# Kernel optimization log

Hardware: AMD Instinct MI355X
Metric: run time of the kernel (lower is better)

Reference implementation:

```python
import jax, jax.numpy as jnp
import numpy as np

N_NODES = 50000
N_EDGES = 800000
ENC_DIM = 128


def setup_inputs() -> dict:
    key = jax.random.key(0)
    k_h, k_s, k_d, k_w1, k_w2 = jax.random.split(key, 5)
    h = jax.random.normal(k_h, (N_NODES, ENC_DIM), dtype=jnp.float32)
    edge_src = jax.random.randint(k_s, (N_EDGES,), 0, N_NODES, dtype=jnp.int32)
    edge_dst = jax.random.randint(k_d, (N_EDGES,), 0, N_NODES, dtype=jnp.int32)
    # Linear(enc_dim*2 -> enc_dim) per layer; scaled init for numerical sanity
    scale = 1.0 / np.sqrt(2 * ENC_DIM)
    W1 = jax.random.normal(k_w1, (2 * ENC_DIM, ENC_DIM), dtype=jnp.float32) * scale
    b1 = jnp.zeros((ENC_DIM,), dtype=jnp.float32)
    W2 = jax.random.normal(k_w2, (2 * ENC_DIM, ENC_DIM), dtype=jnp.float32) * scale
    b2 = jnp.zeros((ENC_DIM,), dtype=jnp.float32)
    return {"h": h, "edge_src": edge_src, "edge_dst": edge_dst,
            "W1": W1, "b1": b1, "W2": W2, "b2": b2}


def _sage_layer(h, edge_src, edge_dst, W, b):
    # mean over neighbor features: segment-sum messages h[src] at dst, divide by degree
    n = h.shape[0]
    msg_sum = jax.ops.segment_sum(h[edge_src], edge_dst, num_segments=n)  # [N, D]
    deg = jax.ops.segment_sum(jnp.ones_like(edge_dst, dtype=h.dtype), edge_dst,
                              num_segments=n)  # [N]
    m = msg_sum / jnp.maximum(deg, 1.0)[:, None]  # zero-neighbor nodes -> zeros
    hc = jnp.concatenate([h, m], axis=1)  # [N, 2D]
    return jax.nn.relu(hc @ W + b)


def reference(h, edge_src, edge_dst, W1, b1, W2, b2):
    h = _sage_layer(h, edge_src, edge_dst, W1, b1)
    h = _sage_layer(h, edge_src, edge_dst, W2, b2)
    return h
```

## Files before the change

kernel.cpp:

```cpp
#include <hip/hip_runtime.h>

#define D 128
#define BKT_SHIFT 9
#define BKT_NODES 512
#define NBK 128
#define CHUNK 2048
#define CAP 12288

typedef short short8 __attribute__((ext_vector_type(8)));
typedef float f32x4  __attribute__((ext_vector_type(4)));

__device__ __forceinline__ unsigned short f2bf(float f) {
    unsigned int u = __builtin_bit_cast(unsigned int, f);
    u += 0x7FFFu + ((u >> 16) & 1u);
    return (unsigned short)(u >> 16);
}
__device__ __forceinline__ float bflo(unsigned int u) {
    return __builtin_bit_cast(float, u << 16);
}
__device__ __forceinline__ float bfhi(unsigned int u) {
    return __builtin_bit_cast(float, u & 0xFFFF0000u);
}

__global__ __launch_bounds__(256) void prep_bucket(
    const float* __restrict__ h, unsigned short* __restrict__ hbf, int n8,
    int hblocks,
    const float* __restrict__ W1, const float* __restrict__ W2,
    unsigned short* __restrict__ wf1, unsigned short* __restrict__ wf2,
    const int* __restrict__ esrc, const int* __restrict__ edst,
    int* __restrict__ cursor, int* __restrict__ adj_st, int n_edges)
{
    const int bid = blockIdx.x;
    const int tid = threadIdx.x;
    if (bid < hblocks) {
        const int t = bid * 256 + tid;
        if (t >= n8) return;
        const float4 a = reinterpret_cast<const float4*>(h)[t * 2];
        const float4 b = reinterpret_cast<const float4*>(h)[t * 2 + 1];
        union { short8 s; unsigned short u[8]; } pk;
        pk.u[0]=f2bf(a.x); pk.u[1]=f2bf(a.y); pk.u[2]=f2bf(a.z); pk.u[3]=f2bf(a.w);
        pk.u[4]=f2bf(b.x); pk.u[5]=f2bf(b.y); pk.u[6]=f2bf(b.z); pk.u[7]=f2bf(b.w);
        reinterpret_cast<short8*>(hbf)[t] = pk.s;
    } else if (bid < hblocks + 32) {
        const int t = (bid - hblocks) * 256 + tid;
        const int which = t >> 12;
        const int u = t & 4095;
        const float* W = which ? W2 : W1;
        unsigned short* wf = which ? wf2 : wf1;
        const int lane = u & 63;
        const int frag = u >> 6;
        const int ctb  = frag >> 3;
        const int kc   = frag & 7;
        const int col  = ctb * 16 + (lane & 15);
        const int k0   = kc * 32 + (lane >> 4) * 8;
        unsigned short o[8];
        #pragma unroll
        for (int j = 0; j < 8; ++j) o[j] = f2bf(W[(size_t)(k0 + j) * D + col]);
        #pragma unroll
        for (int j = 0; j < 8; ++j) wf[(size_t)u * 8 + j] = o[j];
    } else {
        __shared__ int lcnt[NBK], lbase[NBK];
        const int base = (bid - hblocks - 32) * CHUNK;
        if (tid < NBK) lcnt[tid] = 0;
        __syncthreads();
        int d[8], s[8], loc[8];
        #pragma unroll
        for (int k = 0; k < 8; ++k) {
            const int i = base + k * 256 + tid;
            if (i < n_edges) {
                d[k] = edst[i]; s[k] = esrc[i];
                loc[k] = atomicAdd(&lcnt[d[k] >> BKT_SHIFT], 1);
            }
        }
        __syncthreads();
        if (tid < NBK)
            lbase[tid] = tid * CAP +
                (lcnt[tid] ? atomicAdd(&cursor[tid], lcnt[tid]) : 0);
        __syncthreads();
        #pragma unroll
        for (int k = 0; k < 8; ++k) {
            const int i = base + k * 256 + tid;
            if (i < n_edges) {
                const int b = d[k] >> BKT_SHIFT;
                adj_st[lbase[b] + loc[k]] = (int)(
                    ((unsigned int)(d[k] & (BKT_NODES - 1)) << 16) |
                    (unsigned int)s[k]);
            }
        }
    }
}

__global__ __launch_bounds__(256) void bucket_fill(
    const int* __restrict__ cursor, int* __restrict__ adj_st,
    int* __restrict__ row_start, int* __restrict__ deg, int n_nodes)
{
    __shared__ unsigned int lbuf[CAP];
    __shared__ int cnt[BKT_NODES], pref[BKT_NODES], cur[BKT_NODES];
    __shared__ int wsum[4];
    const int b   = blockIdx.x;
    const int tid = threadIdx.x;
    const int nb  = min(cursor[b], CAP);
    const int s0  = b * CAP;

    for (int i = tid; i < nb; i += 256) lbuf[i] = (unsigned int)adj_st[s0 + i];
    for (int i = tid; i < BKT_NODES; i += 256) cnt[i] = 0;
    __syncthreads();
    for (int i = tid; i < nb; i += 256)
        atomicAdd(&cnt[lbuf[i] >> 16], 1);
    __syncthreads();

    const int lane = tid & 63, w = tid >> 6;
    const int v0 = cnt[2 * tid], v1 = cnt[2 * tid + 1];
    const int sv = v0 + v1;
    int incl = sv;
    #pragma unroll
    for (int off = 1; off < 64; off <<= 1) {
        int t = __shfl_up(incl, off, 64);
        if (lane >= off) incl += t;
    }
    if (lane == 63) wsum[w] = incl;
    __syncthreads();
    int wp = 0;
    #pragma unroll
    for (int k = 0; k < 4; ++k) if (k < w) wp += wsum[k];
    const int ex = wp + incl - sv;
    pref[2 * tid] = ex;           cur[2 * tid] = 0;
    pref[2 * tid + 1] = ex + v0;  cur[2 * tid + 1] = 0;
    __syncthreads();

    for (int r = tid; r < BKT_NODES; r += 256) {
        const int node = b * BKT_NODES + r;
        if (node < n_nodes) { row_start[node] = s0 + pref[r]; deg[node] = cnt[r]; }
    }

    for (int i = tid; i < nb; i += 256) {
        const unsigned int p = lbuf[i];
        const int r = p >> 16;
        adj_st[s0 + pref[r] + atomicAdd(&cur[r], 1)] = (int)(p & 0xFFFFu);
    }
}

__global__ __launch_bounds__(256) void gather_sort(
    const unsigned short* __restrict__ hbf, int* __restrict__ adj,
    const int* __restrict__ row_start, const int* __restrict__ deg,
    unsigned short* __restrict__ msgbf, int n_nodes)
{
    const int lane = threadIdx.x & 63;
    const int node = (blockIdx.x * 256 + threadIdx.x) >> 6;
    if (node >= n_nodes) return;
    const unsigned int* h2 = reinterpret_cast<const unsigned int*>(hbf);

    const int s0 = row_start[node];
    const int d  = deg[node];
    float ax0=0.f, ay0=0.f, ax1=0.f, ay1=0.f, ax2=0.f, ay2=0.f, ax3=0.f, ay3=0.f;
    float ax4=0.f, ay4=0.f, ax5=0.f, ay5=0.f, ax6=0.f, ay6=0.f, ax7=0.f, ay7=0.f;

    if (d <= 64) {
        int v = (lane < d) ? adj[s0 + lane] : 0x7FFFFFFF;
        if (d > 1) {
            #pragma unroll
            for (int k = 2; k <= 64; k <<= 1) {
                #pragma unroll
                for (int j = k >> 1; j >= 1; j >>= 1) {
                    const int p = __shfl_xor(v, j, 64);
                    const bool keepMin = (((lane & k) == 0) == ((lane & j) == 0));
                    v = keepMin ? (v < p ? v : p) : (v > p ? v : p);
                }
            }
            if (lane < d) adj[s0 + lane] = v;
        }
        int p = 0;
        for (; p + 7 < d; p += 8) {
            const int i0 = __shfl(v, p),     i1 = __shfl(v, p + 1);
            const int i2 = __shfl(v, p + 2), i3 = __shfl(v, p + 3);
            const int i4 = __shfl(v, p + 4), i5 = __shfl(v, p + 5);
            const int i6 = __shfl(v, p + 6), i7 = __shfl(v, p + 7);
            const unsigned int w0 = h2[(size_t)i0 * 64 + lane];
            const unsigned int w1 = h2[(size_t)i1 * 64 + lane];
            const unsigned int w2 = h2[(size_t)i2 * 64 + lane];
            const unsigned int w3 = h2[(size_t)i3 * 64 + lane];
            const unsigned int w4 = h2[(size_t)i4 * 64 + lane];
            const unsigned int w5 = h2[(size_t)i5 * 64 + lane];
            const unsigned int w6 = h2[(size_t)i6 * 64 + lane];
            const unsigned int w7 = h2[(size_t)i7 * 64 + lane];
            ax0 += bflo(w0); ay0 += bfhi(w0); ax1 += bflo(w1); ay1 += bfhi(w1);
            ax2 += bflo(w2); ay2 += bfhi(w2); ax3 += bflo(w3); ay3 += bfhi(w3);
            ax4 += bflo(w4); ay4 += bfhi(w4); ax5 += bflo(w5); ay5 += bfhi(w5);
            ax6 += bflo(w6); ay6 += bfhi(w6); ax7 += bflo(w7); ay7 += bfhi(w7);
        }
        for (; p < d; ++p) {
            const int i0 = __shfl(v, p);
            const unsigned int a = h2[(size_t)i0 * 64 + lane];
            ax0 += bflo(a); ay0 += bfhi(a);
        }
    } else {
        int p = 0;
        for (; p + 7 < d; p += 8) {
            const int i0 = adj[s0+p],   i1 = adj[s0+p+1], i2 = adj[s0+p+2], i3 = adj[s0+p+3];
            const int i4 = adj[s0+p+4], i5 = adj[s0+p+5], i6 = adj[s0+p+6], i7 = adj[s0+p+7];
            const unsigned int w0 = h2[(size_t)i0 * 64 + lane];
            const unsigned int w1 = h2[(size_t)i1 * 64 + lane];
            const unsigned int w2 = h2[(size_t)i2 * 64 + lane];
            const unsigned int w3 = h2[(size_t)i3 * 64 + lane];
            const unsigned int w4 = h2[(size_t)i4 * 64 + lane];
            const unsigned int w5 = h2[(size_t)i5 * 64 + lane];
            const unsigned int w6 = h2[(size_t)i6 * 64 + lane];
            const unsigned int w7 = h2[(size_t)i7 * 64 + lane];
            ax0 += bflo(w0); ay0 += bfhi(w0); ax1 += bflo(w1); ay1 += bfhi(w1);
            ax2 += bflo(w2); ay2 += bfhi(w2); ax3 += bflo(w3); ay3 += bfhi(w3);
            ax4 += bflo(w4); ay4 += bfhi(w4); ax5 += bflo(w5); ay5 += bfhi(w5);
            ax6 += bflo(w6); ay6 += bfhi(w6); ax7 += bflo(w7); ay7 += bfhi(w7);
        }
        for (; p < d; ++p) {
            const unsigned int a = h2[(size_t)adj[s0 + p] * 64 + lane];
            ax0 += bflo(a); ay0 += bfhi(a);
        }
    }
    const float inv = 1.0f / (float)(d > 0 ? d : 1);
    const float sx = (((ax0 + ax1) + (ax2 + ax3)) + ((ax4 + ax5) + (ax6 + ax7))) * inv;
    const float sy = (((ay0 + ay1) + (ay2 + ay3)) + ((ay4 + ay5) + (ay6 + ay7))) * inv;
    const unsigned int o = (unsigned int)f2bf(sx) | ((unsigned int)f2bf(sy) << 16);
    reinterpret_cast<unsigned int*>(msgbf)[(size_t)node * 64 + lane] = o;
}

__global__ __launch_bounds__(256) void gather_kernel(
    const unsigned short* __restrict__ hbf, const int* __restrict__ adj,
    const int* __restrict__ row_start, const int* __restrict__ deg,
    unsigned short* __restrict__ msgbf, int n_nodes)
{
    const int lane = threadIdx.x & 63;
    const int node = (blockIdx.x * 256 + threadIdx.x) >> 6;
    if (node >= n_nodes) return;
    const unsigned int* h2 = reinterpret_cast<const unsigned int*>(hbf);

    const int s0 = row_start[node];
    const int d  = deg[node];
    const int s1 = s0 + d;
    float ax0=0.f, ay0=0.f, ax1=0.f, ay1=0.f, ax2=0.f, ay2=0.f, ax3=0.f, ay3=0.f;
    float ax4=0.f, ay4=0.f, ax5=0.f, ay5=0.f, ax6=0.f, ay6=0.f, ax7=0.f, ay7=0.f;
    int p = s0;
    for (; p + 7 < s1; p += 8) {
        const int i0 = adj[p],     i1 = adj[p + 1], i2 = adj[p + 2], i3 = adj[p + 3];
        const int i4 = adj[p + 4], i5 = adj[p + 5], i6 = adj[p + 6], i7 = adj[p + 7];
        const unsigned int v0 = h2[(size_t)i0 * 64 + lane];
        const unsigned int v1 = h2[(size_t)i1 * 64 + lane];
        const unsigned int v2 = h2[(size_t)i2 * 64 + lane];
        const unsigned int v3 = h2[(size_t)i3 * 64 + lane];
        const unsigned int v4 = h2[(size_t)i4 * 64 + lane];
        const unsigned int v5 = h2[(size_t)i5 * 64 + lane];
        const unsigned int v6 = h2[(size_t)i6 * 64 + lane];
        const unsigned int v7 = h2[(size_t)i7 * 64 + lane];
        ax0 += bflo(v0); ay0 += bfhi(v0); ax1 += bflo(v1); ay1 += bfhi(v1);
        ax2 += bflo(v2); ay2 += bfhi(v2); ax3 += bflo(v3); ay3 += bfhi(v3);
        ax4 += bflo(v4); ay4 += bfhi(v4); ax5 += bflo(v5); ay5 += bfhi(v5);
        ax6 += bflo(v6); ay6 += bfhi(v6); ax7 += bflo(v7); ay7 += bfhi(v7);
    }
    for (; p + 3 < s1; p += 4) {
        const int i0 = adj[p], i1 = adj[p + 1], i2 = adj[p + 2], i3 = adj[p + 3];
        const unsigned int v0 = h2[(size_t)i0 * 64 + lane];
        const unsigned int v1 = h2[(size_t)i1 * 64 + lane];
        const unsigned int v2 = h2[(size_t)i2 * 64 + lane];
        const unsigned int v3 = h2[(size_t)i3 * 64 + lane];
        ax0 += bflo(v0); ay0 += bfhi(v0); ax1 += bflo(v1); ay1 += bfhi(v1);
        ax2 += bflo(v2); ay2 += bfhi(v2); ax3 += bflo(v3); ay3 += bfhi(v3);
    }
    for (; p < s1; ++p) {
        const unsigned int a = h2[(size_t)adj[p] * 64 + lane];
        ax0 += bflo(a); ay0 += bfhi(a);
    }
    const float inv = 1.0f / (float)(d > 0 ? d : 1);
    const float sx = (((ax0 + ax1) + (ax2 + ax3)) + ((ax4 + ax5) + (ax6 + ax7))) * inv;
    const float sy = (((ay0 + ay1) + (ay2 + ay3)) + ((ay4 + ay5) + (ay6 + ay7))) * inv;
    const unsigned int o = (unsigned int)f2bf(sx) | ((unsigned int)f2bf(sy) << 16);
    reinterpret_cast<unsigned int*>(msgbf)[(size_t)node * 64 + lane] = o;
}

template<bool OUT_BF16>
__global__ __launch_bounds__(256) void gemm_mfma(
    const unsigned short* __restrict__ hbf, const unsigned short* __restrict__ msgbf,
    const unsigned short* __restrict__ wfrag, const float* __restrict__ bias,
    float* __restrict__ outf, unsigned short* __restrict__ outbf, int n_nodes)
{
    __shared__ unsigned short sA[64 * 256];
    const int tid  = threadIdx.x;
    const int base = blockIdx.x * 64;

    #pragma unroll
    for (int it = 0; it < 8; ++it) {
        const int f  = it * 256 + tid;
        const int r  = f >> 5;
        const int cc = f & 31;
        const int node = base + r;
        short8 v = {0,0,0,0,0,0,0,0};
        if (node < n_nodes) {
            const unsigned short* sp = (cc < 16)
                ? hbf   + (size_t)node * D + cc * 8
                : msgbf + (size_t)node * D + (cc - 16) * 8;
            v = *reinterpret_cast<const short8*>(sp);
        }
        *reinterpret_cast<short8*>(&sA[r * 256 + ((cc ^ (r & 7)) * 8)]) = v;
    }
    __syncthreads();

    const int wv   = tid >> 6;
    const int lane = tid & 63;
    const int lrow = wv * 16 + (lane & 15);
    const int lgrp = lane >> 4;

    short8 a[8];
    #pragma unroll
    for (int kc = 0; kc < 8; ++kc) {
        const int chunk = kc * 4 + lgrp;
        a[kc] = *reinterpret_cast<const short8*>(
            &sA[lrow * 256 + ((chunk ^ (lrow & 7)) * 8)]);
    }

    const short8* wf = reinterpret_cast<const short8*>(wfrag);
    f32x4 acc[8];
    #pragma unroll
    for (int ct = 0; ct < 8; ++ct) {
        const float bb = bias[ct * 16 + (lane & 15)];
        acc[ct] = (f32x4){bb, bb, bb, bb};
    }
    #pragma unroll
    for (int ct = 0; ct < 8; ++ct) {
        #pragma unroll
        for (int kc = 0; kc < 8; ++kc) {
            const short8 b = wf[(ct * 8 + kc) * 64 + lane];
            acc[ct] = __builtin_amdgcn_mfma_f32_16x16x32_bf16(a[kc], b, acc[ct], 0, 0, 0);
        }
    }

    #pragma unroll
    for (int ct = 0; ct < 8; ++ct) {
        const int col = ct * 16 + (lane & 15);
        #pragma unroll
        for (int rg = 0; rg < 4; ++rg) {
            const int node = base + wv * 16 + lgrp * 4 + rg;
            if (node < n_nodes) {
                const float r = fmaxf(acc[ct][rg], 0.f);
                if (OUT_BF16) outbf[(size_t)node * D + col] = f2bf(r);
                else          outf [(size_t)node * D + col] = r;
            }
        }
    }
}

extern "C" void kernel_launch(void* const* d_in, const int* in_sizes, int n_in,
                              void* d_out, int out_size, void* d_ws, size_t ws_size,
                              hipStream_t stream)
{
    const float* h    = (const float*)d_in[0];
    const int*   esrc = (const int*)  d_in[1];
    const int*   edst = (const int*)  d_in[2];
    const float* W1   = (const float*)d_in[3];
    const float* b1   = (const float*)d_in[4];
    const float* W2   = (const float*)d_in[5];
    const float* b2   = (const float*)d_in[6];
    float* out = (float*)d_out;

    const int n_nodes = in_sizes[0] / D;
    const int n_edges = in_sizes[1];
    const int nbuck   = (n_nodes + BKT_NODES - 1) >> BKT_SHIFT;

    unsigned short* hbf   = (unsigned short*)d_ws;
    unsigned short* h1bf  = hbf  + (size_t)n_nodes * D;
    unsigned short* msgbf = h1bf + (size_t)n_nodes * D;
    unsigned short* wf1   = msgbf + (size_t)n_nodes * D;
    unsigned short* wf2   = wf1 + 32768;
    int* adj_st           = (int*)(wf2 + 32768);
    int* row_start        = adj_st + (size_t)nbuck * CAP;
    int* deg              = row_start + n_nodes;
    int* cursor           = deg + n_nodes;

    const int nchunks = (n_edges + CHUNK - 1) / CHUNK;
    const int nodewave_blocks = (n_nodes + 3) / 4;
    const int gemm_blocks = (n_nodes + 63) / 64;
    const int n8 = n_nodes * D / 8;
    const int hblocks = (n8 + 255) / 256;

    (void)hipMemsetAsync(cursor, 0, NBK * sizeof(int), stream);
    prep_bucket<<<hblocks + 32 + nchunks, 256, 0, stream>>>(
        h, hbf, n8, hblocks, W1, W2, wf1, wf2, esrc, edst, cursor, adj_st, n_edges);
    bucket_fill<<<nbuck, 256, 0, stream>>>(cursor, adj_st, row_start, deg, n_nodes);

    gather_sort<<<nodewave_blocks, 256, 0, stream>>>(hbf, adj_st, row_start, deg, msgbf, n_nodes);
    gemm_mfma<true><<<gemm_blocks, 256, 0, stream>>>(hbf, msgbf, wf1, b1, nullptr, h1bf, n_nodes);

    gather_kernel<<<nodewave_blocks, 256, 0, stream>>>(h1bf, adj_st, row_start, deg, msgbf, n_nodes);
    gemm_mfma<false><<<gemm_blocks, 256, 0, stream>>>(h1bf, msgbf, wf2, b2, out, nullptr, n_nodes);
}
```

Before: 144.7 us.

## Fuse neighbor gather-mean into MFMA GEMM kernel per layer

Merges the gather (mean aggregation) and the MFMA GEMM into one kernel per layer. Each wave gathers 16 nodes sequentially and writes its own and aggregated features straight into shared memory, so the msgbf round trip through global memory and two kernel launches go away. The cost is less parallelism during the gather: 782 blocks, each wave walking 16 nodes serially, instead of one wave per node across 12500 blocks. The MFMA phase must also wait for the slowest wave's gather, which may hurt latency hiding on the irregular loads.

```diff
diff --git a/kernel.cpp b/kernel.cpp
--- a/kernel.cpp
+++ b/kernel.cpp
@@ -140,22 +140,15 @@
     }
 }
 
-__global__ __launch_bounds__(256) void gather_sort(
-    const unsigned short* __restrict__ hbf, int* __restrict__ adj,
-    const int* __restrict__ row_start, const int* __restrict__ deg,
-    unsigned short* __restrict__ msgbf, int n_nodes)
-{
-    const int lane = threadIdx.x & 63;
-    const int node = (blockIdx.x * 256 + threadIdx.x) >> 6;
-    if (node >= n_nodes) return;
-    const unsigned int* h2 = reinterpret_cast<const unsigned int*>(hbf);
-
-    const int s0 = row_start[node];
-    const int d  = deg[node];
+template<bool SORT>
+__device__ __forceinline__ unsigned int gather_mean(
+    const unsigned int* __restrict__ h2, int* __restrict__ adj,
+    int s0, int d, int lane)
+{
     float ax0=0.f, ay0=0.f, ax1=0.f, ay1=0.f, ax2=0.f, ay2=0.f, ax3=0.f, ay3=0.f;
     float ax4=0.f, ay4=0.f, ax5=0.f, ay5=0.f, ax6=0.f, ay6=0.f, ax7=0.f, ay7=0.f;
 
-    if (d <= 64) {
+    if (SORT && d <= 64) {
         int v = (lane < d) ? adj[s0 + lane] : 0x7FFFFFFF;
         if (d > 1) {
             #pragma unroll
@@ -219,94 +212,41 @@
     const float inv = 1.0f / (float)(d > 0 ? d : 1);
     const float sx = (((ax0 + ax1) + (ax2 + ax3)) + ((ax4 + ax5) + (ax6 + ax7))) * inv;
     const float sy = (((ay0 + ay1) + (ay2 + ay3)) + ((ay4 + ay5) + (ay6 + ay7))) * inv;
-    const unsigned int o = (unsigned int)f2bf(sx) | ((unsigned int)f2bf(sy) << 16);
-    reinterpret_cast<unsigned int*>(msgbf)[(size_t)node * 64 + lane] = o;
-}
-
-__global__ __launch_bounds__(256) void gather_kernel(
-    const unsigned short* __restrict__ hbf, const int* __restrict__ adj,
+    return (unsigned int)f2bf(sx) | ((unsigned int)f2bf(sy) << 16);
+}
+
+template<bool SORT, bool OUT_BF16>
+__global__ __launch_bounds__(256) void fused_layer(
+    const unsigned short* __restrict__ hbf, int* __restrict__ adj,
     const int* __restrict__ row_start, const int* __restrict__ deg,
-    unsigned short* __restrict__ msgbf, int n_nodes)
-{
-    const int lane = threadIdx.x & 63;
-    const int node = (blockIdx.x * 256 + threadIdx.x) >> 6;
-    if (node >= n_nodes) return;
-    const unsigned int* h2 = reinterpret_cast<const unsigned int*>(hbf);
-
-    const int s0 = row_start[node];
-    const int d  = deg[node];
-    const int s1 = s0 + d;
-    float ax0=0.f, ay0=0.f, ax1=0.f, ay1=0.f, ax2=0.f, ay2=0.f, ax3=0.f, ay3=0.f;
-    float ax4=0.f, ay4=0.f, ax5=0.f, ay5=0.f, ax6=0.f, ay6=0.f, ax7=0.f, ay7=0.f;
-    int p = s0;
-    for (; p + 7 < s1; p += 8) {
-        const int i0 = adj[p],     i1 = adj[p + 1], i2 = adj[p + 2], i3 = adj[p + 3];
-        const int i4 = adj[p + 4], i5 = adj[p + 5], i6 = adj[p + 6], i7 = adj[p + 7];
-        const unsigned int v0 = h2[(size_t)i0 * 64 + lane];
-        const unsigned int v1 = h2[(size_t)i1 * 64 + lane];
-        const unsigned int v2 = h2[(size_t)i2 * 64 + lane];
-        const unsigned int v3 = h2[(size_t)i3 * 64 + lane];
-        const unsigned int v4 = h2[(size_t)i4 * 64 + lane];
-        const unsigned int v5 = h2[(size_t)i5 * 64 + lane];
-        const unsigned int v6 = h2[(size_t)i6 * 64 + lane];
-        const unsigned int v7 = h2[(size_t)i7 * 64 + lane];
-        ax0 += bflo(v0); ay0 += bfhi(v0); ax1 += bflo(v1); ay1 += bfhi(v1);
-        ax2 += bflo(v2); ay2 += bfhi(v2); ax3 += bflo(v3); ay3 += bfhi(v3);
-        ax4 += bflo(v4); ay4 += bfhi(v4); ax5 += bflo(v5); ay5 += bfhi(v5);
-        ax6 += bflo(v6); ay6 += bfhi(v6); ax7 += bflo(v7); ay7 += bfhi(v7);
-    }
-    for (; p + 3 < s1; p += 4) {
-        const int i0 = adj[p], i1 = adj[p + 1], i2 = adj[p + 2], i3 = adj[p + 3];
-        const unsigned int v0 = h2[(size_t)i0 * 64 + lane];
-        const unsigned int v1 = h2[(size_t)i1 * 64 + lane];
-        const unsigned int v2 = h2[(size_t)i2 * 64 + lane];
-        const unsigned int v3 = h2[(size_t)i3 * 64 + lane];
-        ax0 += bflo(v0); ay0 += bfhi(v0); ax1 += bflo(v1); ay1 += bfhi(v1);
-        ax2 += bflo(v2); ay2 += bfhi(v2); ax3 += bflo(v3); ay3 += bfhi(v3);
-    }
-    for (; p < s1; ++p) {
-        const unsigned int a = h2[(size_t)adj[p] * 64 + lane];
-        ax0 += bflo(a); ay0 += bfhi(a);
-    }
-    const float inv = 1.0f / (float)(d > 0 ? d : 1);
-    const float sx = (((ax0 + ax1) + (ax2 + ax3)) + ((ax4 + ax5) + (ax6 + ax7))) * inv;
-    const float sy = (((ay0 + ay1) + (ay2 + ay3)) + ((ay4 + ay5) + (ay6 + ay7))) * inv;
-    const unsigned int o = (unsigned int)f2bf(sx) | ((unsigned int)f2bf(sy) << 16);
-    reinterpret_cast<unsigned int*>(msgbf)[(size_t)node * 64 + lane] = o;
-}
-
-template<bool OUT_BF16>
-__global__ __launch_bounds__(256) void gemm_mfma(
-    const unsigned short* __restrict__ hbf, const unsigned short* __restrict__ msgbf,
     const unsigned short* __restrict__ wfrag, const float* __restrict__ bias,
     float* __restrict__ outf, unsigned short* __restrict__ outbf, int n_nodes)
 {
     __shared__ unsigned short sA[64 * 256];
+    unsigned int* sA32 = reinterpret_cast<unsigned int*>(sA);
     const int tid  = threadIdx.x;
-    const int base = blockIdx.x * 64;
-
-    #pragma unroll
-    for (int it = 0; it < 8; ++it) {
-        const int f  = it * 256 + tid;
-        const int r  = f >> 5;
-        const int cc = f & 31;
-        const int node = base + r;
-        short8 v = {0,0,0,0,0,0,0,0};
-        if (node < n_nodes) {
-            const unsigned short* sp = (cc < 16)
-                ? hbf   + (size_t)node * D + cc * 8
-                : msgbf + (size_t)node * D + (cc - 16) * 8;
-            v = *reinterpret_cast<const short8*>(sp);
-        }
-        *reinterpret_cast<short8*>(&sA[r * 256 + ((cc ^ (r & 7)) * 8)]) = v;
-    }
-    __syncthreads();
-
     const int wv   = tid >> 6;
     const int lane = tid & 63;
+    const int base = blockIdx.x * 64;
+    const unsigned int* h2 = reinterpret_cast<const unsigned int*>(hbf);
+
+    const int cco = lane >> 2;
+    const int sub = lane & 3;
+    for (int i = 0; i < 16; ++i) {
+        const int r    = wv * 16 + i;
+        const int node = base + r;
+        unsigned int own = 0, msg = 0;
+        if (node < n_nodes) {
+            own = h2[(size_t)node * 64 + lane];
+            msg = gather_mean<SORT>(h2, adj, row_start[node], deg[node], lane);
+        }
+        sA32[r * 128 + (((cco     ) ^ (r & 7)) << 2) + sub] = own;
+        sA32[r * 128 + (((cco + 16) ^ (r & 7)) << 2) + sub] = msg;
+    }
+    __syncthreads();
+
     const int lrow = wv * 16 + (lane & 15);
     const int lgrp = lane >> 4;
-
     short8 a[8];
     #pragma unroll
     for (int kc = 0; kc < 8; ++kc) {
@@ -365,8 +305,7 @@
 
     unsigned short* hbf   = (unsigned short*)d_ws;
     unsigned short* h1bf  = hbf  + (size_t)n_nodes * D;
-    unsigned short* msgbf = h1bf + (size_t)n_nodes * D;
-    unsigned short* wf1   = msgbf + (size_t)n_nodes * D;
+    unsigned short* wf1   = h1bf + (size_t)n_nodes * D;
     unsigned short* wf2   = wf1 + 32768;
     int* adj_st           = (int*)(wf2 + 32768);
     int* row_start        = adj_st + (size_t)nbuck * CAP;
@@ -374,8 +313,7 @@
     int* cursor           = deg + n_nodes;
 
     const int nchunks = (n_edges + CHUNK - 1) / CHUNK;
-    const int nodewave_blocks = (n_nodes + 3) / 4;
-    const int gemm_blocks = (n_nodes + 63) / 64;
+    const int layer_blocks = (n_nodes + 63) / 64;
     const int n8 = n_nodes * D / 8;
     const int hblocks = (n8 + 255) / 256;
 
@@ -384,9 +322,9 @@
         h, hbf, n8, hblocks, W1, W2, wf1, wf2, esrc, edst, cursor, adj_st, n_edges);
     bucket_fill<<<nbuck, 256, 0, stream>>>(cursor, adj_st, row_start, deg, n_nodes);
 
-    gather_sort<<<nodewave_blocks, 256, 0, stream>>>(hbf, adj_st, row_start, deg, msgbf, n_nodes);
-    gemm_mfma<true><<<gemm_blocks, 256, 0, stream>>>(hbf, msgbf, wf1, b1, nullptr, h1bf, n_nodes);
-
-    gather_kernel<<<nodewave_blocks, 256, 0, stream>>>(h1bf, adj_st, row_start, deg, msgbf, n_nodes);
-    gemm_mfma<false><<<gemm_blocks, 256, 0, stream>>>(h1bf, msgbf, wf2, b2, out, nullptr, n_nodes);
-}
+    fused_layer<true, true><<<layer_blocks, 256, 0, stream>>>(
+        hbf, adj_st, row_start, deg, wf1, b1, nullptr, h1bf, n_nodes);
+
+    fused_layer<false, false><<<layer_blocks, 256, 0, stream>>>(
+        h1bf, adj_st, row_start, deg, wf2, b2, out, nullptr, n_nodes);
+}
```

Measured after the change: 190.6 us. 31.7% more time.
